# Performance work log

Measured on AMD Instinct MI355X. Metric: run time of the kernel, lower is better.

## Reference

```python
import jax, jax.numpy as jnp
import numpy as np

RES = 256      # cubic grid resolution
CH = 16        # feature channels
RR = 8         # reduced_res = ceil(log2(RES))
MASK = 128     # low-frequency mask size
N_PTS = 262144 # query points


def _bilinear(feat, gx, gy):
    """torch.F.grid_sample, bilinear, align_corners=True, zero padding.
    feat: (C,H,W); gx,gy: (N,) in [-1,1] (gx indexes W, gy indexes H).
    Returns (N,C)."""
    H, W = feat.shape[1], feat.shape[2]
    x = (gx + 1.0) * 0.5 * (W - 1)
    y = (gy + 1.0) * 0.5 * (H - 1)
    x0 = jnp.floor(x)
    y0 = jnp.floor(y)
    wx = x - x0
    wy = y - y0
    x0i = jnp.clip(x0.astype(jnp.int32), 0, W - 1)
    x1i = jnp.clip(x0i + 1, 0, W - 1)
    y0i = jnp.clip(y0.astype(jnp.int32), 0, H - 1)
    y1i = jnp.clip(y0i + 1, 0, H - 1)
    v00 = feat[:, y0i, x0i]
    v01 = feat[:, y0i, x1i]
    v10 = feat[:, y1i, x0i]
    v11 = feat[:, y1i, x1i]
    out = (v00 * (1 - wx) * (1 - wy) + v01 * wx * (1 - wy)
           + v10 * (1 - wx) * wy + v11 * wx * wy)  # (C,N)
    return out.T


def _plane(P, mask2d, gx, gy, icoord):
    """One phasor plane: mask -> ifft2 -> grid_sample -> Fourier integration.
    P: (CH*RR, RES, RES, 2); returns (N, CH)."""
    Pc = (P[..., 0] + 1j * P[..., 1]) * mask2d          # (C,H,W) complex
    Pc = jnp.fft.ifft2(Pc)                              # ifft over last 2 axes
    C = P.shape[0]
    # interleave (real, imag) per complex channel, like permute+reshape in torch
    feat = jnp.stack([Pc.real, Pc.imag], axis=1).reshape(2 * C, RES, RES)
    samp = _bilinear(feat, gx, gy).reshape(-1, 2 * CH, RR)  # (N, 2*CH, RR)
    Z = samp[:, :CH] + 1j * samp[:, CH:]                    # (N, CH, RR)
    s = (icoord + 1.0) * 0.5 * (2 ** RR - 1)                # scaled coord
    coef = 2.0 ** jnp.arange(RR) - 1.0                      # (RR,)
    basis = jnp.exp(2j * jnp.pi * s[:, None] * coef / (2 ** RR))  # (N, RR)
    return jnp.einsum('nr,ncr->nc', basis, Z).real


def _forward(Pu, Pv, Pw, inputs):
    mask2d = jnp.zeros((RES, RES), jnp.float32).at[:MASK, :MASK].set(1.0)
    out = (_plane(Pu, mask2d, inputs[:, 1], inputs[:, 2], inputs[:, 0])
           + _plane(Pv, mask2d, inputs[:, 0], inputs[:, 2], inputs[:, 1])
           + _plane(Pw, mask2d, inputs[:, 0], inputs[:, 1], inputs[:, 2]))
    return out  # (N, CH)


def setup_inputs() -> dict:
    key = jax.random.key(0)
    k1, k2, k3, k4 = jax.random.split(key, 4)
    Pu = 0.001 * jax.random.normal(k1, (CH * RR, RES, RES, 2), jnp.float32)
    Pv = 0.001 * jax.random.normal(k2, (CH * RR, RES, RES, 2), jnp.float32)
    Pw = 0.001 * jax.random.normal(k3, (CH * RR, RES, RES, 2), jnp.float32)
    inputs = jax.random.uniform(k4, (N_PTS, 3), jnp.float32, -1.0, 1.0)
    return {"Pu": Pu, "Pv": Pv, "Pw": Pw, "inputs": inputs}


def reference(Pu, Pv, Pw, inputs):
    return _forward(Pu, Pv, Pw, inputs)
```

## Files before the change

### kernel.cpp

```cpp
#include <hip/hip_runtime.h>
#include <hip/hip_bf16.h>
#include <cmath>


#define NPTS 262144

typedef float vf2 __attribute__((ext_vector_type(2)));

__device__ __forceinline__ int brev8(int x) { return (int)(__brev((unsigned)x) >> 24); }

__device__ __forceinline__ unsigned pack_bf16(float2 v) {
    unsigned short a = __builtin_bit_cast(unsigned short, __float2bfloat16(v.x));
    unsigned short b = __builtin_bit_cast(unsigned short, __float2bfloat16(v.y));
    return (unsigned)a | ((unsigned)b << 16);
}
__device__ __forceinline__ float2 unpack_bf16(unsigned u) {
    return make_float2(__uint_as_float(u << 16), __uint_as_float(u & 0xffff0000u));
}
__device__ __forceinline__ vf2 up2(unsigned u) {
    vf2 r; r.x = __uint_as_float(u << 16); r.y = __uint_as_float(u & 0xffff0000u);
    return r;
}

__device__ __forceinline__ void plane_coords(int p, float in0, float in1, float in2,
                                             float& gx, float& gy, float& sc) {
    gx = (p == 0) ? in1 : in0;
    gy = (p == 2) ? in1 : in2;
    sc = (p == 0) ? in0 : ((p == 1) ? in1 : in2);
}

__global__ __launch_bounds__(512) void pass1_kernel(const float* __restrict__ P0,
                                                    const float* __restrict__ P1,
                                                    const float* __restrict__ P2,
                                                    unsigned* __restrict__ X) {
    __shared__ float2 tw[128];
    __shared__ float2 tile[256 * 17];

    int t = threadIdx.x;
    if (t < 128) {
        float s, c;
        sincospif((float)t * (1.0f / 128.0f), &s, &c);
        tw[t] = make_float2(c, s);
    }
    int plane = blockIdx.y;
    const float* P = (plane == 0) ? P0 : ((plane == 1) ? P1 : P2);
    unsigned* Xp = X + (size_t)plane * 4194304;

    int b  = blockIdx.x;
    int ch = b >> 3;
    int x0 = (b & 7) << 4;
    const float* src = P + (size_t)ch * 131072 + x0 * 2;

    const float scale = 1.0f / 65536.0f;
#pragma unroll
    for (int k = 0; k < 2; k++) {
        int i = t + (k << 9);
        int y = i >> 3;
        int j = i & 7;
        float4 v = *(const float4*)(src + (size_t)y * 512 + (j << 2));
        float2 c0 = make_float2(v.x * scale, v.y * scale);
        float2 c1 = make_float2(v.z * scale, v.w * scale);
        int pos = brev8(y);
        tile[pos * 17 + 2 * j]           = c0;
        tile[(pos + 1) * 17 + 2 * j]     = c0;
        tile[pos * 17 + 2 * j + 1]       = c1;
        tile[(pos + 1) * 17 + 2 * j + 1] = c1;
    }
    __syncthreads();

    int w = t >> 6, l = t & 63;
    int col = (w << 1) + (l & 1);
    int bb  = l >> 1;
#pragma unroll
    for (int s = 2; s <= 8; s++) {
        int half = 1 << (s - 1);
#pragma unroll
        for (int k = 0; k < 4; k++) {
            int bf = bb + (k << 5);
            int j  = bf & (half - 1);
            int g  = bf >> (s - 1);
            int i0 = (g << s) + j;
            int i1 = i0 + half;
            float2 u = tile[i0 * 17 + col];
            float2 v = tile[i1 * 17 + col];
            float2 wq = tw[j << (8 - s)];
            float2 vt = make_float2(v.x * wq.x - v.y * wq.y, v.x * wq.y + v.y * wq.x);
            tile[i0 * 17 + col] = make_float2(u.x + vt.x, u.y + vt.y);
            tile[i1 * 17 + col] = make_float2(u.x - vt.x, u.y - vt.y);
        }
    }
    __syncthreads();

    unsigned* dst = Xp + (size_t)ch * 32768 + x0;
#pragma unroll
    for (int k = 0; k < 8; k++) {
        int i = t + (k << 9);
        int v = i >> 4;
        int c = i & 15;
        dst[(size_t)v * 128 + c] = pack_bf16(tile[v * 17 + c]);
    }
}

__global__ __launch_bounds__(1024) void pass2_kernel(const unsigned* __restrict__ X,
                                                     __hip_bfloat16* __restrict__ feat) {
    __shared__ float2 tw[128];
    __shared__ float2 rows[16 * 257];

    int t = threadIdx.x;
    if (t < 128) {
        float s, c;
        sincospif((float)t * (1.0f / 128.0f), &s, &c);
        tw[t] = make_float2(c, s);
    }
    int w = t >> 6;
    int l = t & 63;
    int v   = blockIdx.x & 255;
    int g   = blockIdx.x >> 8;
    int ch0 = g << 4;
    int ch  = ch0 + w;
    int plane = blockIdx.y;
    const unsigned* Xp = X + (size_t)plane * 4194304;
    __hip_bfloat16* fp = feat + (size_t)plane * 16777216;

    const uint2* src = (const uint2*)(Xp + ((size_t)ch * 256 + v) * 128);
    uint2 d = src[l];
    float2 c0 = unpack_bf16(d.x);
    float2 c1 = unpack_bf16(d.y);
    float2* row = rows + w * 257;
    int p0 = brev8(2 * l);
    int p1 = brev8(2 * l + 1);
    row[p0]     = c0;
    row[p0 + 1] = c0;
    row[p1]     = c1;
    row[p1 + 1] = c1;
    __syncthreads();
#pragma unroll
    for (int s = 2; s <= 8; s++) {
        int half = 1 << (s - 1);
#pragma unroll
        for (int k = 0; k < 2; k++) {
            int bf = l + (k << 6);
            int j  = bf & (half - 1);
            int gg = bf >> (s - 1);
            int i0 = (gg << s) + j;
            int i1 = i0 + half;
            float2 u  = row[i0];
            float2 vv = row[i1];
            float2 wq = tw[j << (8 - s)];
            float2 vt = make_float2(vv.x * wq.x - vv.y * wq.y,
                                    vv.x * wq.y + vv.y * wq.x);
            row[i0] = make_float2(u.x + vt.x, u.y + vt.y);
            row[i1] = make_float2(u.x - vt.x, u.y - vt.y);
        }
    }
    __syncthreads();
    __hip_bfloat16* dst = fp + (size_t)v * 65536 + (ch0 << 1);
#pragma unroll
    for (int k = 0; k < 8; k++) {
        int f = t + (k << 10);
        int x = f >> 5;
        int j = f & 31;
        float2 cpx = rows[(j >> 1) * 257 + x];
        float val = (j & 1) ? cpx.y : cpx.x;
        dst[x * 256 + j] = __float2bfloat16(val);
    }
}

__device__ __forceinline__ int tile_key(float gx, float gy) {
    float xf = (gx + 1.0f) * 127.5f;
    float yf = (gy + 1.0f) * 127.5f;
    int x0 = max(0, min((int)floorf(xf), 255));
    int y0 = max(0, min((int)floorf(yf), 255));
    return (y0 & 0xF0) | (x0 >> 4);
}

__global__ __launch_bounds__(1024) void hist_kernel(const float* __restrict__ pts,
                                                    unsigned* __restrict__ hist) {
    __shared__ unsigned hb[256];
    int t = threadIdx.x;
    int p = blockIdx.y;
    int n = (blockIdx.x << 10) + t;
    if (t < 256) hb[t] = 0;
    __syncthreads();
    float in0 = pts[3 * n + 0], in1 = pts[3 * n + 1], in2 = pts[3 * n + 2];
    float gx, gy, sc;
    plane_coords(p, in0, in1, in2, gx, gy, sc);
    atomicAdd(&hb[tile_key(gx, gy)], 1u);
    __syncthreads();
    if (t < 256 && hb[t]) atomicAdd(&hist[(p << 8) + t], hb[t]);
}

__global__ __launch_bounds__(256) void scan_kernel(const unsigned* __restrict__ hist,
                                                   unsigned* __restrict__ cursor) {
    __shared__ unsigned s[256];
    int t = threadIdx.x;
    for (int p = 0; p < 3; p++) {
        unsigned v = hist[(p << 8) + t];
        s[t] = v;
        __syncthreads();
#pragma unroll
        for (int d = 1; d < 256; d <<= 1) {
            unsigned add = (t >= d) ? s[t - d] : 0u;
            __syncthreads();
            s[t] += add;
            __syncthreads();
        }
        cursor[(p << 8) + t] = s[t] - v;
        __syncthreads();
    }
}

__global__ __launch_bounds__(1024) void scatter_kernel(const float* __restrict__ pts,
                                                       unsigned* __restrict__ cursor,
                                                       float4* __restrict__ psort) {
    __shared__ unsigned cnt[256];
    __shared__ unsigned base[256];
    int t = threadIdx.x;
    int p = blockIdx.y;
    int n = (blockIdx.x << 10) + t;
    if (t < 256) cnt[t] = 0;
    __syncthreads();
    float in0 = pts[3 * n + 0], in1 = pts[3 * n + 1], in2 = pts[3 * n + 2];
    float gx, gy, sc;
    plane_coords(p, in0, in1, in2, gx, gy, sc);
    int key = tile_key(gx, gy);
    unsigned rank = atomicAdd(&cnt[key], 1u);
    __syncthreads();
    if (t < 256 && cnt[t]) base[t] = atomicAdd(&cursor[(p << 8) + t], cnt[t]);
    __syncthreads();
    psort[p * NPTS + base[key] + rank] = make_float4(gx, gy, sc, __int_as_float(n));
}

__global__ __launch_bounds__(256) void gather_kernel(const ushort* __restrict__ feat,
                                                     const float4* __restrict__ psort,
                                                     float* __restrict__ partial) {
    int t = threadIdx.x;
    int w = t >> 6;
    int l = t & 63;
    int h = l >> 5;
    int q = l & 31;
    int p = blockIdx.y;
    const ushort* fb = feat + (size_t)p * 16777216;

    int b  = blockIdx.x;
    int lb = ((b & 7) << 12) | (b >> 3);
    int idx = (lb << 3) + (w << 1) + h;
    float4 pt = psort[p * NPTS + idx];
    float gx = pt.x, gy = pt.y, sc = pt.z;
    int n = __float_as_int(pt.w);

    float xf = (gx + 1.0f) * 127.5f;
    float yf = (gy + 1.0f) * 127.5f;
    float x0f = floorf(xf);
    float y0f = floorf(yf);
    float wx = xf - x0f;
    float wy = yf - y0f;
    int x0 = max(0, min((int)x0f, 255));
    int y0 = max(0, min((int)y0f, 255));
    int dx = (x0 < 255) ? 256 : 0;
    int dy = (y0 < 255) ? 65536 : 0;

    const ushort* bp = fb + (((y0 << 8) + x0) << 8) + (q << 3);
    uint4 d00 = *(const uint4*)bp;
    uint4 d01 = *(const uint4*)(bp + dx);
    uint4 d10 = *(const uint4*)(bp + dy);
    uint4 d11 = *(const uint4*)(bp + dx + dy);

    float coef = (float)((1 << (q & 7)) - 1);
    float a = (sc + 1.0f) * 0.99609375f * coef;
    float sn, cs;
    sincospif(a, &sn, &cs);
    float merged = (q < 16) ? cs : -sn;
    float wr0 = __shfl(merged, (l & 48) + 0);
    float wr1 = __shfl(merged, (l & 48) + 1);
    float wr2 = __shfl(merged, (l & 48) + 2);
    float wr3 = __shfl(merged, (l & 48) + 3);
    float wr4 = __shfl(merged, (l & 48) + 4);
    float wr5 = __shfl(merged, (l & 48) + 5);
    float wr6 = __shfl(merged, (l & 48) + 6);
    float wr7 = __shfl(merged, (l & 48) + 7);

    float w00 = (1.0f - wx) * (1.0f - wy);
    float w01 = wx * (1.0f - wy);
    float w10 = (1.0f - wx) * wy;
    float w11 = wx * wy;

    vf2 b0 = w00 * up2(d00.x) + w01 * up2(d01.x) + w10 * up2(d10.x) + w11 * up2(d11.x);
    vf2 b1 = w00 * up2(d00.y) + w01 * up2(d01.y) + w10 * up2(d10.y) + w11 * up2(d11.y);
    vf2 b2 = w00 * up2(d00.z) + w01 * up2(d01.z) + w10 * up2(d10.z) + w11 * up2(d11.z);
    vf2 b3 = w00 * up2(d00.w) + w01 * up2(d01.w) + w10 * up2(d10.w) + w11 * up2(d11.w);

    vf2 wa; wa.x = wr0; wa.y = wr1;
    vf2 wb; wb.x = wr2; wb.y = wr3;
    vf2 wc; wc.x = wr4; wc.y = wr5;
    vf2 wd; wd.x = wr6; wd.y = wr7;
    vf2 acc2 = b0 * wa + b1 * wb + b2 * wc + b3 * wd;
    float acc = acc2.x + acc2.y;

    acc += __shfl_xor(acc, 16);
    if (q < 16) {
        partial[(((size_t)p * NPTS + n) << 4) + q] = acc;
    }
}

__global__ __launch_bounds__(256) void combine_kernel(const float4* __restrict__ pa,
                                                      float4* __restrict__ out) {
    int i = (blockIdx.x << 8) + threadIdx.x;
    float4 a = pa[i];
    float4 b = pa[i + 1048576];
    float4 c = pa[i + 2097152];
    out[i] = make_float4(a.x + b.x + c.x, a.y + b.y + c.y,
                         a.z + b.z + c.z, a.w + b.w + c.w);
}

extern "C" void kernel_launch(void* const* d_in, const int* in_sizes, int n_in,
                              void* d_out, int out_size, void* d_ws, size_t ws_size,
                              hipStream_t stream) {
    const float* P0  = (const float*)d_in[0];
    const float* P1  = (const float*)d_in[1];
    const float* P2  = (const float*)d_in[2];
    const float* pts = (const float*)d_in[3];
    float* out = (float*)d_out;
    char* ws = (char*)d_ws;

    __hip_bfloat16* feat = (__hip_bfloat16*)ws;
    unsigned* X          = (unsigned*)(ws + 100663296u);
    float*    partial    = (float*)(ws + 150994944u);
    float4*   psort      = (float4*)(ws + 201326592u);
    unsigned* hist       = (unsigned*)(ws + 213909504u);
    unsigned* cursor     = (unsigned*)(ws + 213912576u);

    hipMemsetAsync(hist, 0, 3072, stream);

    dim3 g1(1024, 3);
    pass1_kernel<<<g1, 512, 0, stream>>>(P0, P1, P2, X);
    dim3 g2(2048, 3);
    pass2_kernel<<<g2, 1024, 0, stream>>>(X, feat);

    dim3 gs(256, 3);
    hist_kernel<<<gs, 1024, 0, stream>>>(pts, hist);
    scan_kernel<<<1, 256, 0, stream>>>(hist, cursor);
    scatter_kernel<<<gs, 1024, 0, stream>>>(pts, cursor, psort);

    dim3 gg(32768, 3);
    gather_kernel<<<gg, 256, 0, stream>>>((const ushort*)feat, psort, partial);
    combine_kernel<<<4096, 256, 0, stream>>>((const float4*)partial, (float4*)out);
}
```

Measured before the change: 395.7 us.

## Vectorize FFT output stores, merge plane loops in hist/scatter, atomically accumulate output

New measurement: 404.0 us. 1.02x slower.

```diff
diff --git a/kernel.cpp b/kernel.cpp
--- a/kernel.cpp
+++ b/kernel.cpp
@@ -92,12 +92,18 @@
     __syncthreads();
 
     unsigned* dst = Xp + (size_t)ch * 32768 + x0;
-#pragma unroll
-    for (int k = 0; k < 8; k++) {
-        int i = t + (k << 9);
-        int v = i >> 4;
-        int c = i & 15;
-        dst[(size_t)v * 128 + c] = pack_bf16(tile[v * 17 + c]);
+    int c4 = (t & 3) << 2;
+    int v0 = t >> 2;
+#pragma unroll
+    for (int k = 0; k < 2; k++) {
+        int v = v0 + (k << 7);
+        const float2* tp = &tile[v * 17 + c4];
+        uint4 o;
+        o.x = pack_bf16(tp[0]);
+        o.y = pack_bf16(tp[1]);
+        o.z = pack_bf16(tp[2]);
+        o.w = pack_bf16(tp[3]);
+        *(uint4*)(dst + (size_t)v * 128 + c4) = o;
     }
 }
 
@@ -154,16 +160,17 @@
         }
     }
     __syncthreads();
+
     __hip_bfloat16* dst = fp + (size_t)v * 65536 + (ch0 << 1);
-#pragma unroll
-    for (int k = 0; k < 8; k++) {
-        int f = t + (k << 10);
-        int x = f >> 5;
-        int j = f & 31;
-        float2 cpx = rows[(j >> 1) * 257 + x];
-        float val = (j & 1) ? cpx.y : cpx.x;
-        dst[x * 256 + j] = __float2bfloat16(val);
-    }
+    int j8  = (t & 3) << 3;
+    int x   = t >> 2;
+    int jj0 = j8 >> 1;
+    uint4 o;
+    o.x = pack_bf16(rows[(jj0 + 0) * 257 + x]);
+    o.y = pack_bf16(rows[(jj0 + 1) * 257 + x]);
+    o.z = pack_bf16(rows[(jj0 + 2) * 257 + x]);
+    o.w = pack_bf16(rows[(jj0 + 3) * 257 + x]);
+    *(uint4*)(dst + x * 256 + j8) = o;
 }
 
 __device__ __forceinline__ int tile_key(float gx, float gy) {
@@ -176,18 +183,20 @@
 
 __global__ __launch_bounds__(1024) void hist_kernel(const float* __restrict__ pts,
                                                     unsigned* __restrict__ hist) {
-    __shared__ unsigned hb[256];
-    int t = threadIdx.x;
-    int p = blockIdx.y;
+    __shared__ unsigned hb[768];
+    int t = threadIdx.x;
     int n = (blockIdx.x << 10) + t;
-    if (t < 256) hb[t] = 0;
+    if (t < 768) hb[t] = 0;
     __syncthreads();
     float in0 = pts[3 * n + 0], in1 = pts[3 * n + 1], in2 = pts[3 * n + 2];
-    float gx, gy, sc;
-    plane_coords(p, in0, in1, in2, gx, gy, sc);
-    atomicAdd(&hb[tile_key(gx, gy)], 1u);
-    __syncthreads();
-    if (t < 256 && hb[t]) atomicAdd(&hist[(p << 8) + t], hb[t]);
+#pragma unroll
+    for (int p = 0; p < 3; p++) {
+        float gx, gy, sc;
+        plane_coords(p, in0, in1, in2, gx, gy, sc);
+        atomicAdd(&hb[(p << 8) + tile_key(gx, gy)], 1u);
+    }
+    __syncthreads();
+    if (t < 768 && hb[t]) atomicAdd(&hist[t], hb[t]);
 }
 
 __global__ __launch_bounds__(256) void scan_kernel(const unsigned* __restrict__ hist,
@@ -213,27 +222,35 @@
 __global__ __launch_bounds__(1024) void scatter_kernel(const float* __restrict__ pts,
                                                        unsigned* __restrict__ cursor,
                                                        float4* __restrict__ psort) {
-    __shared__ unsigned cnt[256];
-    __shared__ unsigned base[256];
-    int t = threadIdx.x;
-    int p = blockIdx.y;
+    __shared__ unsigned cnt[768];
+    __shared__ unsigned base[768];
+    int t = threadIdx.x;
     int n = (blockIdx.x << 10) + t;
-    if (t < 256) cnt[t] = 0;
+    if (t < 768) cnt[t] = 0;
     __syncthreads();
     float in0 = pts[3 * n + 0], in1 = pts[3 * n + 1], in2 = pts[3 * n + 2];
-    float gx, gy, sc;
-    plane_coords(p, in0, in1, in2, gx, gy, sc);
-    int key = tile_key(gx, gy);
-    unsigned rank = atomicAdd(&cnt[key], 1u);
-    __syncthreads();
-    if (t < 256 && cnt[t]) base[t] = atomicAdd(&cursor[(p << 8) + t], cnt[t]);
-    __syncthreads();
-    psort[p * NPTS + base[key] + rank] = make_float4(gx, gy, sc, __int_as_float(n));
+    float gxs[3], gys[3], scs[3];
+    int key[3];
+    unsigned rank[3];
+#pragma unroll
+    for (int p = 0; p < 3; p++) {
+        plane_coords(p, in0, in1, in2, gxs[p], gys[p], scs[p]);
+        key[p] = (p << 8) + tile_key(gxs[p], gys[p]);
+        rank[p] = atomicAdd(&cnt[key[p]], 1u);
+    }
+    __syncthreads();
+    if (t < 768 && cnt[t]) base[t] = atomicAdd(&cursor[t], cnt[t]);
+    __syncthreads();
+#pragma unroll
+    for (int p = 0; p < 3; p++) {
+        psort[p * NPTS + base[key[p]] + rank[p]] =
+            make_float4(gxs[p], gys[p], scs[p], __int_as_float(n));
+    }
 }
 
 __global__ __launch_bounds__(256) void gather_kernel(const ushort* __restrict__ feat,
                                                      const float4* __restrict__ psort,
-                                                     float* __restrict__ partial) {
+                                                     float* __restrict__ out) {
     int t = threadIdx.x;
     int w = t >> 6;
     int l = t & 63;
@@ -299,18 +316,8 @@
 
     acc += __shfl_xor(acc, 16);
     if (q < 16) {
-        partial[(((size_t)p * NPTS + n) << 4) + q] = acc;
-    }
-}
-
-__global__ __launch_bounds__(256) void combine_kernel(const float4* __restrict__ pa,
-                                                      float4* __restrict__ out) {
-    int i = (blockIdx.x << 8) + threadIdx.x;
-    float4 a = pa[i];
-    float4 b = pa[i + 1048576];
-    float4 c = pa[i + 2097152];
-    out[i] = make_float4(a.x + b.x + c.x, a.y + b.y + c.y,
-                         a.z + b.z + c.z, a.w + b.w + c.w);
+        atomicAdd(&out[((size_t)n << 4) + q], acc);
+    }
 }
 
 extern "C" void kernel_launch(void* const* d_in, const int* in_sizes, int n_in,
@@ -325,24 +332,22 @@
 
     __hip_bfloat16* feat = (__hip_bfloat16*)ws;
     unsigned* X          = (unsigned*)(ws + 100663296u);
-    float*    partial    = (float*)(ws + 150994944u);
-    float4*   psort      = (float4*)(ws + 201326592u);
-    unsigned* hist       = (unsigned*)(ws + 213909504u);
-    unsigned* cursor     = (unsigned*)(ws + 213912576u);
+    float4*   psort      = (float4*)(ws + 150994944u);
+    unsigned* hist       = (unsigned*)(ws + 163577856u);
+    unsigned* cursor     = (unsigned*)(ws + 163580928u);
 
     hipMemsetAsync(hist, 0, 3072, stream);
+    hipMemsetAsync(out, 0, (size_t)out_size * sizeof(float), stream);
 
     dim3 g1(1024, 3);
     pass1_kernel<<<g1, 512, 0, stream>>>(P0, P1, P2, X);
     dim3 g2(2048, 3);
     pass2_kernel<<<g2, 1024, 0, stream>>>(X, feat);
 
-    dim3 gs(256, 3);
-    hist_kernel<<<gs, 1024, 0, stream>>>(pts, hist);
+    hist_kernel<<<256, 1024, 0, stream>>>(pts, hist);
     scan_kernel<<<1, 256, 0, stream>>>(hist, cursor);
-    scatter_kernel<<<gs, 1024, 0, stream>>>(pts, cursor, psort);
+    scatter_kernel<<<256, 1024, 0, stream>>>(pts, cursor, psort);
 
     dim3 gg(32768, 3);
-    gather_kernel<<<gg, 256, 0, stream>>>((const ushort*)feat, psort, partial);
-    combine_kernel<<<4096, 256, 0, stream>>>((const float4*)partial, (float4*)out);
-}
+    gather_kernel<<<gg, 256, 0, stream>>>((const ushort*)feat, psort, out);
+}
```
